# Performance work log

Measured on AMD Instinct MI355X. Metric: run time of the kernel, lower is better.

The kernel has to match this reference:

```python
import jax, jax.numpy as jnp
import numpy as np

N_RAY, N_SAMPLES = 131072, 128
BIG_DELTA = 1e10
EPS = 1e-10


def setup_inputs() -> dict:
    key = jax.random.key(0)
    k1, k2, k3 = jax.random.split(key, 3)
    rgb = jax.random.uniform(k1, (N_RAY, N_SAMPLES, 3), dtype=jnp.float32)
    sigma = jax.random.normal(k2, (N_RAY, N_SAMPLES), dtype=jnp.float32)
    # sorted depths per ray in [2.0, 6.0), mimicking near/far bounds
    z_raw = jax.random.uniform(k3, (N_RAY, N_SAMPLES), dtype=jnp.float32, minval=2.0, maxval=6.0)
    z_vals = jnp.sort(z_raw, axis=-1)
    return {"rgb": rgb, "sigma": sigma, "z_vals": z_vals, "white_bkgd": 1}


def reference(rgb, sigma, z_vals, white_bkgd):
    # deltas: distance between adjacent samples, last one set to a huge value
    deltas = z_vals[:, 1:] - z_vals[:, :-1]
    deltas = jnp.concatenate(
        [deltas, jnp.full_like(deltas[:, :1], BIG_DELTA)], axis=-1)
    # sigma_activation = relu (opt.sigma_activation == 'relu')
    alpha = 1.0 - jnp.exp(-deltas * jax.nn.relu(sigma))
    # exclusive cumulative product of transmittance
    accum_prod = jnp.concatenate(
        [jnp.ones_like(alpha[:, :1]),
         jnp.cumprod(1.0 - alpha[:, :-1] + EPS, axis=-1)], axis=-1)
    weights = alpha * accum_prod                    # [N_ray, N_samples]
    comp_rgb = jnp.einsum('ns,nsc->nc', weights, rgb)  # [N_ray, 3]
    depth = jnp.sum(weights * z_vals, axis=-1)         # [N_ray]
    opacity = jnp.sum(weights, axis=-1)                # [N_ray]
    if white_bkgd:
        comp_rgb = comp_rgb + (1.0 - opacity[:, None])
    return comp_rgb, depth, opacity, weights
```

## Files before the change

kernel.cpp:

```cpp
#include <hip/hip_runtime.h>

#define N_RAY 131072
#define NS 128
#define BIG_DELTA 1e10f
#define EPS 1e-10f

__global__ __launch_bounds__(256) void volrender_kernel(
    const float4* __restrict__ rgb4,
    const float4* __restrict__ sigma4,
    const float4* __restrict__ z4,
    const int* __restrict__ wb_flag,
    float* __restrict__ out)
{
    const int tid = blockIdx.x * blockDim.x + threadIdx.x;
    const int ray = tid >> 5;
    const int l   = threadIdx.x & 31;
    if (ray >= N_RAY) return;

    const float4 z = z4[(size_t)ray * 32 + l];
    const float4 s = sigma4[(size_t)ray * 32 + l];

    float z_next = __shfl_down(z.x, 1, 32);
    float d0 = z.y - z.x;
    float d1 = z.z - z.y;
    float d2 = z.w - z.z;
    float d3 = (l == 31) ? BIG_DELTA : (z_next - z.w);

    float a0 = 1.0f - __expf(-d0 * fmaxf(s.x, 0.0f));
    float a1 = 1.0f - __expf(-d1 * fmaxf(s.y, 0.0f));
    float a2 = 1.0f - __expf(-d2 * fmaxf(s.z, 0.0f));
    float a3 = 1.0f - __expf(-d3 * fmaxf(s.w, 0.0f));

    float t0 = 1.0f - a0 + EPS;
    float t1 = 1.0f - a1 + EPS;
    float t2 = 1.0f - a2 + EPS;
    float t3 = 1.0f - a3 + EPS;

    float p = (t0 * t1) * (t2 * t3);
    #pragma unroll
    for (int d = 1; d < 32; d <<= 1) {
        float q = __shfl_up(p, d, 32);
        if (l >= d) p *= q;
    }
    float e = __shfl_up(p, 1, 32);
    if (l == 0) e = 1.0f;

    float w0 = a0 * e;
    float e1 = e * t0;
    float w1 = a1 * e1;
    float e2 = e1 * t1;
    float w2 = a2 * e2;
    float w3 = a3 * (e2 * t2);

    float4* wout = reinterpret_cast<float4*>(out + (size_t)N_RAY * 5) + (size_t)ray * 32 + l;
    *wout = make_float4(w0, w1, w2, w3);

    const float4* rp = rgb4 + (size_t)ray * 96 + 3 * l;
    float4 c0 = rp[0];
    float4 c1 = rp[1];
    float4 c2 = rp[2];

    float r   = w0 * c0.x + w1 * c0.w + w2 * c1.z + w3 * c2.y;
    float g   = w0 * c0.y + w1 * c1.x + w2 * c1.w + w3 * c2.z;
    float b   = w0 * c0.z + w1 * c1.y + w2 * c2.x + w3 * c2.w;
    float dep = w0 * z.x  + w1 * z.y  + w2 * z.z  + w3 * z.w;
    float op  = w0 + w1 + w2 + w3;

    #pragma unroll
    for (int d = 16; d > 0; d >>= 1) {
        r   += __shfl_down(r,   d, 32);
        g   += __shfl_down(g,   d, 32);
        b   += __shfl_down(b,   d, 32);
        dep += __shfl_down(dep, d, 32);
        op  += __shfl_down(op,  d, 32);
    }

    if (l == 0) {
        const int wb = *wb_flag;
        const float add = wb ? (1.0f - op) : 0.0f;
        out[(size_t)ray * 3 + 0] = r + add;
        out[(size_t)ray * 3 + 1] = g + add;
        out[(size_t)ray * 3 + 2] = b + add;
        out[(size_t)N_RAY * 3 + ray] = dep;
        out[(size_t)N_RAY * 4 + ray] = op;
    }
}

extern "C" void kernel_launch(void* const* d_in, const int* in_sizes, int n_in,
                              void* d_out, int out_size, void* d_ws, size_t ws_size,
                              hipStream_t stream) {
    const float4* rgb    = (const float4*)d_in[0];
    const float4* sigma  = (const float4*)d_in[1];
    const float4* z_vals = (const float4*)d_in[2];
    const int*    wb     = (const int*)d_in[3];
    float* out = (float*)d_out;

    const int blocks = (N_RAY * 32) / 256;
    volrender_kernel<<<blocks, 256, 0, stream>>>(rgb, sigma, z_vals, wb, out);
}
```

Measured before the change: 79.40 us.

## Stage ray inputs in LDS via direct global-to-LDS loads, 8 lanes per ray

```diff
diff --git a/kernel.cpp b/kernel.cpp
--- a/kernel.cpp
+++ b/kernel.cpp
@@ -1,86 +1,142 @@
 #include <hip/hip_runtime.h>
+#include <stdint.h>
 
 #define N_RAY 131072
 #define NS 128
 #define BIG_DELTA 1e10f
 #define EPS 1e-10f
+#define RAYS_PB 8
 
-__global__ __launch_bounds__(256) void volrender_kernel(
+__device__ __forceinline__ void gload16(const void* g, void* l) {
+    __builtin_amdgcn_global_load_lds(
+        (const __attribute__((address_space(1))) void*)g,
+        (__attribute__((address_space(3))) void*)l, 16, 0, 0);
+}
+
+__global__ __launch_bounds__(64) void volrender_kernel(
     const float4* __restrict__ rgb4,
     const float4* __restrict__ sigma4,
     const float4* __restrict__ z4,
     const int* __restrict__ wb_flag,
     float* __restrict__ out)
 {
-    const int tid = blockIdx.x * blockDim.x + threadIdx.x;
-    const int ray = tid >> 5;
-    const int l   = threadIdx.x & 31;
-    if (ray >= N_RAY) return;
+    __shared__ float4 zt[32 * 8];
+    __shared__ float4 st[32 * 8];
+    __shared__ float4 ct[96 * 8];
 
-    const float4 z = z4[(size_t)ray * 32 + l];
-    const float4 s = sigma4[(size_t)ray * 32 + l];
+    const int lane = threadIdx.x;
+    const int rayBase = blockIdx.x * RAYS_PB;
 
-    float z_next = __shfl_down(z.x, 1, 32);
-    float d0 = z.y - z.x;
-    float d1 = z.z - z.y;
-    float d2 = z.w - z.z;
-    float d3 = (l == 31) ? BIG_DELTA : (z_next - z.w);
+    const int sr = lane & 7;
+    const int sh = lane >> 3;
 
-    float a0 = 1.0f - __expf(-d0 * fmaxf(s.x, 0.0f));
-    float a1 = 1.0f - __expf(-d1 * fmaxf(s.y, 0.0f));
-    float a2 = 1.0f - __expf(-d2 * fmaxf(s.z, 0.0f));
-    float a3 = 1.0f - __expf(-d3 * fmaxf(s.w, 0.0f));
+    const size_t zb = (size_t)rayBase * 32;
+    #pragma unroll
+    for (int k = 0; k < 4; ++k)
+        gload16(&z4[zb + (size_t)sr * 32 + (k * 8 + sh)], &zt[k * 64]);
+    #pragma unroll
+    for (int k = 0; k < 4; ++k)
+        gload16(&sigma4[zb + (size_t)sr * 32 + (k * 8 + sh)], &st[k * 64]);
+    const size_t cbase = (size_t)rayBase * 96;
+    #pragma unroll
+    for (int k = 0; k < 12; ++k)
+        gload16(&rgb4[cbase + (size_t)sr * 96 + (k * 8 + sh)], &ct[k * 64]);
 
-    float t0 = 1.0f - a0 + EPS;
-    float t1 = 1.0f - a1 + EPS;
-    float t2 = 1.0f - a2 + EPS;
-    float t3 = 1.0f - a3 + EPS;
+    asm volatile("s_waitcnt vmcnt(0)" ::: "memory");
+    __syncthreads();
 
-    float p = (t0 * t1) * (t2 * t3);
+    const int rc = lane >> 3;
+    const int u  = lane & 7;
+
+    float zz[17], ss[16];
     #pragma unroll
-    for (int d = 1; d < 32; d <<= 1) {
-        float q = __shfl_up(p, d, 32);
-        if (l >= d) p *= q;
+    for (int k = 0; k < 4; ++k) {
+        float4 v = zt[(4 * u + k) * 8 + rc];
+        zz[4 * k + 0] = v.x; zz[4 * k + 1] = v.y;
+        zz[4 * k + 2] = v.z; zz[4 * k + 3] = v.w;
+        float4 s = st[(4 * u + k) * 8 + rc];
+        ss[4 * k + 0] = s.x; ss[4 * k + 1] = s.y;
+        ss[4 * k + 2] = s.z; ss[4 * k + 3] = s.w;
     }
-    float e = __shfl_up(p, 1, 32);
-    if (l == 0) e = 1.0f;
+    zz[16] = zt[((u < 7) ? (4 * u + 4) : 31) * 8 + rc].x;
 
-    float w0 = a0 * e;
-    float e1 = e * t0;
-    float w1 = a1 * e1;
-    float e2 = e1 * t1;
-    float w2 = a2 * e2;
-    float w3 = a3 * (e2 * t2);
+    float a[16], t[16];
+    #pragma unroll
+    for (int j = 0; j < 16; ++j) {
+        float dd = (j == 15) ? ((u == 7) ? BIG_DELTA : (zz[16] - zz[15]))
+                             : (zz[j + 1] - zz[j]);
+        float sg = fmaxf(ss[j], 0.0f);
+        a[j] = 1.0f - __expf(-dd * sg);
+        t[j] = 1.0f - a[j] + EPS;
+    }
 
-    float4* wout = reinterpret_cast<float4*>(out + (size_t)N_RAY * 5) + (size_t)ray * 32 + l;
-    *wout = make_float4(w0, w1, w2, w3);
+    float p01, p23, p45, p67;
+    p01 = (t[0] * t[1]) * (t[2] * t[3]);
+    p23 = (t[4] * t[5]) * (t[6] * t[7]);
+    p45 = (t[8] * t[9]) * (t[10] * t[11]);
+    p67 = (t[12] * t[13]) * (t[14] * t[15]);
+    float p = (p01 * p23) * (p45 * p67);
 
-    const float4* rp = rgb4 + (size_t)ray * 96 + 3 * l;
-    float4 c0 = rp[0];
-    float4 c1 = rp[1];
-    float4 c2 = rp[2];
+    float sc = p;
+    #pragma unroll
+    for (int d = 1; d < 8; d <<= 1) {
+        float qv = __shfl_up(sc, d, 8);
+        if (u >= d) sc *= qv;
+    }
+    float e = __shfl_up(sc, 1, 8);
+    if (u == 0) e = 1.0f;
 
-    float r   = w0 * c0.x + w1 * c0.w + w2 * c1.z + w3 * c2.y;
-    float g   = w0 * c0.y + w1 * c1.x + w2 * c1.w + w3 * c2.z;
-    float b   = w0 * c0.z + w1 * c1.y + w2 * c2.x + w3 * c2.w;
-    float dep = w0 * z.x  + w1 * z.y  + w2 * z.z  + w3 * z.w;
-    float op  = w0 + w1 + w2 + w3;
+    float w[16];
+    float E = e, dep = 0.0f, op = 0.0f;
+    #pragma unroll
+    for (int j = 0; j < 16; ++j) {
+        w[j] = a[j] * E;
+        E *= t[j];
+        dep += w[j] * zz[j];
+        op  += w[j];
+    }
+
+    {
+        float4* wq = reinterpret_cast<float4*>(out + (size_t)N_RAY * 5);
+        size_t wbase = ((size_t)(rayBase + rc)) * 32 + 4 * u;
+        #pragma unroll
+        for (int k = 0; k < 4; ++k)
+            wq[wbase + k] = make_float4(w[4 * k], w[4 * k + 1], w[4 * k + 2], w[4 * k + 3]);
+    }
+
+    float cr = 0.0f, cg = 0.0f, cb = 0.0f;
+    #pragma unroll
+    for (int j = 0; j < 12; ++j) {
+        float4 c = ct[(12 * u + j) * 8 + rc];
+        const int f = 4 * j;
+        const int s0 = f / 3;
+        if ((f % 3) == 0) {
+            cr += c.x * w[s0]; cg += c.y * w[s0];
+            cb += c.z * w[s0]; cr += c.w * w[s0 + 1];
+        } else if ((f % 3) == 1) {
+            cg += c.x * w[s0]; cb += c.y * w[s0];
+            cr += c.z * w[s0 + 1]; cg += c.w * w[s0 + 1];
+        } else {
+            cb += c.x * w[s0]; cr += c.y * w[s0 + 1];
+            cg += c.z * w[s0 + 1]; cb += c.w * w[s0 + 1];
+        }
+    }
 
     #pragma unroll
-    for (int d = 16; d > 0; d >>= 1) {
-        r   += __shfl_down(r,   d, 32);
-        g   += __shfl_down(g,   d, 32);
-        b   += __shfl_down(b,   d, 32);
-        dep += __shfl_down(dep, d, 32);
-        op  += __shfl_down(op,  d, 32);
+    for (int d = 4; d >= 1; d >>= 1) {
+        cr  += __shfl_down(cr,  d, 8);
+        cg  += __shfl_down(cg,  d, 8);
+        cb  += __shfl_down(cb,  d, 8);
+        dep += __shfl_down(dep, d, 8);
+        op  += __shfl_down(op,  d, 8);
     }
 
-    if (l == 0) {
-        const int wb = *wb_flag;
-        const float add = wb ? (1.0f - op) : 0.0f;
-        out[(size_t)ray * 3 + 0] = r + add;
-        out[(size_t)ray * 3 + 1] = g + add;
-        out[(size_t)ray * 3 + 2] = b + add;
+    if (u == 0) {
+        const int ray = rayBase + rc;
+        const float add = (*wb_flag) ? (1.0f - op) : 0.0f;
+        out[(size_t)ray * 3 + 0] = cr + add;
+        out[(size_t)ray * 3 + 1] = cg + add;
+        out[(size_t)ray * 3 + 2] = cb + add;
         out[(size_t)N_RAY * 3 + ray] = dep;
         out[(size_t)N_RAY * 4 + ray] = op;
     }
@@ -95,6 +151,6 @@
     const int*    wb     = (const int*)d_in[3];
     float* out = (float*)d_out;
 
-    const int blocks = (N_RAY * 32) / 256;
-    volrender_kernel<<<blocks, 256, 0, stream>>>(rgb, sigma, z_vals, wb, out);
+    const int blocks = N_RAY / RAYS_PB;
+    volrender_kernel<<<blocks, 64, 0, stream>>>(rgb, sigma, z_vals, wb, out);
 }
```

Result: no change. 80.14 us (+0.9%).
